# Kernel optimization log

Measured on AMD Instinct MI355X. Metric: run time of the kernel, lower is better.

The kernel has to match this reference:

```python
import jax, jax.numpy as jnp
import numpy as np

B, T, D = 2, 1024, 2048
E, K, H = 64, 4, 512          # n_experts, top-k, expert_dim
S, HS = 2, H * K              # shared experts, shared hidden dim
CAP = 512


def setup_inputs() -> dict:
    key = jax.random.key(0)
    ks = jax.random.split(key, 9)
    scale = 0.02
    return {
        "x": jax.random.normal(ks[0], (B, T, D), jnp.float32),
        "Wr": jax.random.normal(ks[1], (D, E), jnp.float32) * scale,
        "router_bias": jnp.zeros((E,), jnp.float32),
        "Wg": jax.random.normal(ks[2], (E, D, H), jnp.float32) * scale,
        "Wu": jax.random.normal(ks[3], (E, D, H), jnp.float32) * scale,
        "Wd": jax.random.normal(ks[4], (E, H, D), jnp.float32) * scale,
        "Sg": jax.random.normal(ks[5], (S, D, HS), jnp.float32) * scale,
        "Su": jax.random.normal(ks[6], (S, D, HS), jnp.float32) * scale,
        "Sd": jax.random.normal(ks[7], (S, HS, D), jnp.float32) * scale,
    }


def reference(x, Wr, router_bias, Wg, Wu, Wd, Sg, Su, Sd):
    Bx, Tx, Dx = x.shape
    N = Bx * Tx
    flat = x.reshape(N, Dx)                              # [N, D]

    # ---- router ----
    logits = flat @ Wr + router_bias                     # [N, E]
    scores = jax.nn.softmax(logits, axis=-1)
    topk_scores, topk_idx = jax.lax.top_k(scores, K)     # [N, K]
    topk_scores = topk_scores / topk_scores.sum(-1, keepdims=True)

    eid = topk_idx.reshape(-1)                           # [N*K] expert per assignment
    w = topk_scores.reshape(-1)                          # [N*K] combine weight
    tok = jnp.repeat(jnp.arange(N), K)                   # [N*K] source token id

    # position of each assignment within its expert's buffer
    oh = jax.nn.one_hot(eid, E, dtype=jnp.int32)         # [N*K, E]
    pos = ((jnp.cumsum(oh, axis=0) * oh).sum(-1) - 1)    # [N*K]
    valid = pos < CAP

    # ---- dispatch: scatter tokens into per-expert buffers ----
    xb = jnp.zeros((E, CAP, Dx), x.dtype).at[eid, pos].set(flat[tok], mode="drop")

    # ---- grouped SwiGLU expert FFN ----
    h = jax.nn.silu(jnp.einsum("ecd,edh->ech", xb, Wg)) * jnp.einsum("ecd,edh->ech", xb, Wu)
    yb = jnp.einsum("ech,ehd->ecd", h, Wd)               # [E, CAP, D]

    # ---- combine: gather back and weighted scatter-add to tokens ----
    y = yb[eid, jnp.minimum(pos, CAP - 1)] * (w * valid)[:, None]
    out = jnp.zeros((N, Dx), x.dtype).at[tok].add(y)

    # ---- always-on shared experts ----
    hs = jax.nn.silu(jnp.einsum("nd,sdh->nsh", flat, Sg)) * jnp.einsum("nd,sdh->nsh", flat, Su)
    out = out + jnp.einsum("nsh,shd->nd", hs, Sd)

    return out.reshape(Bx, Tx, Dx)
```

## Files before the change

### kernel.cpp

```cpp
#include <hip/hip_runtime.h>
#include <hip/hip_bf16.h>
#include <stdint.h>

#define N_TOK 2048
#define DM    2048
#define NEXP  64
#define TOPK  4
#define HEXP  512
#define CAPC  512
#define NSH   2
#define HSH   2048
#define RTB   8

typedef __attribute__((ext_vector_type(8))) short short8;
typedef __attribute__((ext_vector_type(4))) short short4v;
typedef __attribute__((ext_vector_type(4))) float f32x4;
typedef __attribute__((ext_vector_type(4))) float f4;

static __device__ __forceinline__ unsigned short f2bf(float f) {
  union { float f; unsigned u; } v; v.f = f;
  unsigned r = v.u + 0x7FFFu + ((v.u >> 16) & 1u);
  return (unsigned short)(r >> 16);
}

__global__ __launch_bounds__(256) void k_convert(const float* __restrict__ x,
                                                 unsigned short* __restrict__ xb) {
  int i = (blockIdx.x * 256 + threadIdx.x) * 8;
  f4 a = *(const f4*)(x + i);
  f4 b = *(const f4*)(x + i + 4);
  short8 o;
  o[0]=f2bf(a[0]); o[1]=f2bf(a[1]); o[2]=f2bf(a[2]); o[3]=f2bf(a[3]);
  o[4]=f2bf(b[0]); o[5]=f2bf(b[1]); o[6]=f2bf(b[2]); o[7]=f2bf(b[3]);
  *(short8*)(xb + i) = o;
}

#define ARGMAX_ROUND(S,I)                                            \
  { float bv = v; int bi = lane;                                     \
    _Pragma("unroll")                                                \
    for (int o = 32; o; o >>= 1) {                                   \
      float ov = __shfl_xor(bv, o); int oi = __shfl_xor(bi, o);      \
      if (ov > bv || (ov == bv && oi < bi)) { bv = ov; bi = oi; }    \
    }                                                                \
    S = bv; I = bi; if (lane == bi) v = -1.f; }

__global__ __launch_bounds__(256) void k_router(const float* __restrict__ x,
    const float* __restrict__ Wr, const float* __restrict__ bias,
    int* __restrict__ cnt, int* __restrict__ lists, float* __restrict__ wlist) {
  __shared__ float part[4][RTB][64];
  __shared__ float logits[RTB][64];
  int t = threadIdx.x;
  int e = t & 63, sl = t >> 6;
  int tok0 = blockIdx.x * RTB;
  const float* xp = x + (size_t)tok0 * DM;
  float acc[RTB];
#pragma unroll
  for (int i = 0; i < RTB; ++i) acc[i] = 0.f;
  for (int d = sl * 512; d < sl * 512 + 512; ++d) {
    float w = Wr[(size_t)d * NEXP + e];
#pragma unroll
    for (int i = 0; i < RTB; ++i) acc[i] += xp[(size_t)i * DM + d] * w;
  }
#pragma unroll
  for (int i = 0; i < RTB; ++i) part[sl][i][e] = acc[i];
  __syncthreads();
  for (int i = sl; i < RTB; i += 4)
    logits[i][e] = part[0][i][e] + part[1][i][e] + part[2][i][e] + part[3][i][e] + bias[e];
  __syncthreads();
  int lane = t & 63, wv = t >> 6;
  for (int i = wv * 2; i < wv * 2 + 2; ++i) {
    float lg = logits[i][lane];
    float m = lg;
#pragma unroll
    for (int o = 32; o; o >>= 1) m = fmaxf(m, __shfl_xor(m, o));
    float p = expf(lg - m);
    float sm = p;
#pragma unroll
    for (int o = 32; o; o >>= 1) sm += __shfl_xor(sm, o);
    float v = p / sm;
    float s0, s1, s2, s3; int i0, i1, i2, i3;
    ARGMAX_ROUND(s0, i0)
    ARGMAX_ROUND(s1, i1)
    ARGMAX_ROUND(s2, i2)
    ARGMAX_ROUND(s3, i3)
    float tot = s0 + s1 + s2 + s3;
    if (lane < TOPK) {
      float myw = (lane == 0 ? s0 : lane == 1 ? s1 : lane == 2 ? s2 : s3) / tot;
      int   mye = (lane == 0 ? i0 : lane == 1 ? i1 : lane == 2 ? i2 : i3);
      int pos = atomicAdd(&cnt[mye], 1);
      if (pos < CAPC) {
        lists[mye * CAPC + pos] = tok0 + i;
        wlist[mye * CAPC + pos] = myw;
      }
    }
  }
}

__global__ void k_offs(const int* __restrict__ cnt, int* __restrict__ offs) {
  int l = threadIdx.x;
  int c = min(cnt[l], CAPC);
  int sum = c;
#pragma unroll
  for (int o = 1; o < 64; o <<= 1) {
    int ov = __shfl_up(sum, o);
    if (l >= o) sum += ov;
  }
  offs[l + 1] = sum;
  if (l == 0) offs[0] = 0;
}


template<bool GATHER>
static __device__ __forceinline__ void loadA(const unsigned short* __restrict__ src,
    int lda, int m0, int Mvalid, const int* __restrict__ gl, int k0, short8 (&r)[4]) {
  int tid = threadIdx.x;
#pragma unroll
  for (int p = 0; p < 4; ++p) {
    int idx = p * 256 + tid;
    int row = idx >> 3;
    int ko  = (idx & 7) * 8;
    int grow = m0 + row;
    if (grow < Mvalid) {
      int srow = GATHER ? gl[grow] : grow;
      r[p] = *(const short8*)(src + (size_t)srow * lda + k0 + ko);
    } else {
#pragma unroll
      for (int j = 0; j < 8; ++j) r[p][j] = 0;
    }
  }
}

static __device__ __forceinline__ void writeA(const short8 (&r)[4], unsigned short* lA) {
  int tid = threadIdx.x;
#pragma unroll
  for (int p = 0; p < 4; ++p) {
    int idx = p * 256 + tid;
    int row = idx >> 3;
    int ko  = (idx & 7) * 8;
    int byte = row * 128 + ko * 2;
    byte ^= (row & 7) << 4;
    *(short8*)((char*)lA + byte) = r[p];
  }
}

static __device__ __forceinline__ void loadB(const float* __restrict__ B, int ldb,
    int k0, int n0, f4 (&r)[4]) {
  int tid = threadIdx.x;
  int kb = tid >> 4;
  int nb = tid & 15;
  const float* p = B + (size_t)(k0 + kb * 4) * ldb + n0 + nb * 4;
#pragma unroll
  for (int q = 0; q < 4; ++q) r[q] = *(const f4*)(p + (size_t)q * ldb);
}

static __device__ __forceinline__ void writeB(const f4 (&r)[4], unsigned short* lB) {
  int tid = threadIdx.x;
  int kb = tid >> 4;
  int nb = tid & 15;
#pragma unroll
  for (int c = 0; c < 4; ++c) {
    short4v vv;
    vv[0] = (short)f2bf(r[0][c]); vv[1] = (short)f2bf(r[1][c]);
    vv[2] = (short)f2bf(r[2][c]); vv[3] = (short)f2bf(r[3][c]);
    int n = nb * 4 + c;
    int byte = n * 128 + kb * 8;
    byte ^= (n & 7) << 4;
    *(short4v*)((char*)lB + byte) = vv;
  }
}

static __device__ __forceinline__ short8 frag_ld(const unsigned short* lds, int row, int kElem) {
  int byte = row * 128 + kElem * 2;
  byte ^= (row & 7) << 4;
  return *(const short8*)((const char*)lds + byte);
}

static __device__ __forceinline__ void mma1(const unsigned short* lA, const unsigned short* lB,
    f32x4 (&acc)[4][2], int wm, int wn, int lane) {
  int r16 = lane & 15;
  int kg  = (lane >> 4) * 8;
#pragma unroll
  for (int kk = 0; kk < 2; ++kk) {
    int kb = kk * 32 + kg;
    short8 a[4], b[2];
#pragma unroll
    for (int mf = 0; mf < 4; ++mf) a[mf] = frag_ld(lA, wm + mf * 16 + r16, kb);
#pragma unroll
    for (int nf = 0; nf < 2; ++nf) b[nf] = frag_ld(lB, wn + nf * 16 + r16, kb);
#pragma unroll
    for (int mf = 0; mf < 4; ++mf)
#pragma unroll
      for (int nf = 0; nf < 2; ++nf)
        acc[mf][nf] = __builtin_amdgcn_mfma_f32_16x16x32_bf16(a[mf], b[nf], acc[mf][nf], 0, 0, 0);
  }
}

static __device__ __forceinline__ void mma2(const unsigned short* lA,
    const unsigned short* lBg, const unsigned short* lBu,
    f32x4 (&accg)[4][2], f32x4 (&accu)[4][2], int wm, int wn, int lane) {
  int r16 = lane & 15;
  int kg  = (lane >> 4) * 8;
#pragma unroll
  for (int kk = 0; kk < 2; ++kk) {
    int kb = kk * 32 + kg;
    short8 a[4], bg[2], bu[2];
#pragma unroll
    for (int mf = 0; mf < 4; ++mf) a[mf] = frag_ld(lA, wm + mf * 16 + r16, kb);
#pragma unroll
    for (int nf = 0; nf < 2; ++nf) {
      bg[nf] = frag_ld(lBg, wn + nf * 16 + r16, kb);
      bu[nf] = frag_ld(lBu, wn + nf * 16 + r16, kb);
    }
#pragma unroll
    for (int mf = 0; mf < 4; ++mf)
#pragma unroll
      for (int nf = 0; nf < 2; ++nf) {
        accg[mf][nf] = __builtin_amdgcn_mfma_f32_16x16x32_bf16(a[mf], bg[nf], accg[mf][nf], 0, 0, 0);
        accu[mf][nf] = __builtin_amdgcn_mfma_f32_16x16x32_bf16(a[mf], bu[nf], accu[mf][nf], 0, 0, 0);
      }
  }
}

static __device__ __forceinline__ float silu_mul(float g, float u) {
  return g / (1.f + expf(-g)) * u;
}

__global__ __launch_bounds__(256) void k_expert_gateup(const unsigned short* __restrict__ xbf,
    const float* __restrict__ Wg, const float* __restrict__ Wu,
    const int* __restrict__ cnt, const int* __restrict__ offs,
    const int* __restrict__ lists, unsigned short* __restrict__ hws) {
  int e = blockIdx.y;
  int ne = min(cnt[e], CAPC);
  if (ne == 0) return;
  int n0 = blockIdx.x * 64;
  const float* Bg = Wg + (size_t)e * DM * HEXP;
  const float* Bu = Wu + (size_t)e * DM * HEXP;
  const int* lst = lists + e * CAPC;
  int base = offs[e];
  __shared__ unsigned short lA[128 * 64];
  __shared__ unsigned short lBg[64 * 64];
  __shared__ unsigned short lBu[64 * 64];
  int lane = threadIdx.x & 63, wv = threadIdx.x >> 6;
  int wm = (wv >> 1) * 64, wn = (wv & 1) * 32;
  for (int m0 = 0; m0 < ne; m0 += 128) {
    f32x4 accg[4][2] = {};
    f32x4 accu[4][2] = {};
    short8 ra[4]; f4 rg[4], ru[4];
    loadA<true>(xbf, DM, m0, ne, lst, 0, ra);
    loadB(Bg, HEXP, 0, n0, rg);
    loadB(Bu, HEXP, 0, n0, ru);
    for (int k0 = 0; k0 < DM; k0 += 64) {
      writeA(ra, lA);
      writeB(rg, lBg);
      writeB(ru, lBu);
      int kn = k0 + 64;
      if (kn < DM) {
        loadA<true>(xbf, DM, m0, ne, lst, kn, ra);
        loadB(Bg, HEXP, kn, n0, rg);
        loadB(Bu, HEXP, kn, n0, ru);
      }
      __syncthreads();
      mma2(lA, lBg, lBu, accg, accu, wm, wn, lane);
      __syncthreads();
    }
#pragma unroll
    for (int mf = 0; mf < 4; ++mf)
#pragma unroll
      for (int r = 0; r < 4; ++r) {
        int rl = m0 + wm + mf * 16 + (lane >> 4) * 4 + r;
        if (rl < ne) {
#pragma unroll
          for (int nf = 0; nf < 2; ++nf) {
            int col = n0 + wn + nf * 16 + (lane & 15);
            float h = silu_mul(accg[mf][nf][r], accu[mf][nf][r]);
            hws[(size_t)(base + rl) * HEXP + col] = f2bf(h);
          }
        }
      }
  }
}

__global__ __launch_bounds__(256) void k_shared_gateup(const unsigned short* __restrict__ xbf,
    const float* __restrict__ Sg, const float* __restrict__ Su,
    unsigned short* __restrict__ hs) {
  int n0 = blockIdx.x * 64;
  int m0 = blockIdx.y * 128;
  int s  = blockIdx.z;
  const float* Bg = Sg + (size_t)s * DM * HSH;
  const float* Bu = Su + (size_t)s * DM * HSH;
  __shared__ unsigned short lA[128 * 64];
  __shared__ unsigned short lBg[64 * 64];
  __shared__ unsigned short lBu[64 * 64];
  int lane = threadIdx.x & 63, wv = threadIdx.x >> 6;
  int wm = (wv >> 1) * 64, wn = (wv & 1) * 32;
  f32x4 accg[4][2] = {};
  f32x4 accu[4][2] = {};
  short8 ra[4]; f4 rg[4], ru[4];
  loadA<false>(xbf, DM, m0, N_TOK, nullptr, 0, ra);
  loadB(Bg, HSH, 0, n0, rg);
  loadB(Bu, HSH, 0, n0, ru);
  for (int k0 = 0; k0 < DM; k0 += 64) {
    writeA(ra, lA);
    writeB(rg, lBg);
    writeB(ru, lBu);
    int kn = k0 + 64;
    if (kn < DM) {
      loadA<false>(xbf, DM, m0, N_TOK, nullptr, kn, ra);
      loadB(Bg, HSH, kn, n0, rg);
      loadB(Bu, HSH, kn, n0, ru);
    }
    __syncthreads();
    mma2(lA, lBg, lBu, accg, accu, wm, wn, lane);
    __syncthreads();
  }
#pragma unroll
  for (int mf = 0; mf < 4; ++mf)
#pragma unroll
    for (int nf = 0; nf < 2; ++nf)
#pragma unroll
      for (int r = 0; r < 4; ++r) {
        int row = m0 + wm + mf * 16 + (lane >> 4) * 4 + r;
        int col = n0 + wn + nf * 16 + (lane & 15);
        float h = silu_mul(accg[mf][nf][r], accu[mf][nf][r]);
        hs[(size_t)row * (NSH * HSH) + s * HSH + col] = f2bf(h);
      }
}

__global__ __launch_bounds__(256) void k_shared_down(const unsigned short* __restrict__ hs,
    const float* __restrict__ Sd, float* __restrict__ out) {
  int n0 = blockIdx.x * 64;
  int m0 = blockIdx.y * 128;
  __shared__ unsigned short lA[128 * 64];
  __shared__ unsigned short lB[64 * 64];
  int lane = threadIdx.x & 63, wv = threadIdx.x >> 6;
  int wm = (wv >> 1) * 64, wn = (wv & 1) * 32;
  f32x4 acc[4][2] = {};
  short8 ra[4]; f4 rb[4];
  loadA<false>(hs, NSH * HSH, m0, N_TOK, nullptr, 0, ra);
  loadB(Sd, DM, 0, n0, rb);
  for (int k0 = 0; k0 < NSH * HSH; k0 += 64) {
    writeA(ra, lA);
    writeB(rb, lB);
    int kn = k0 + 64;
    if (kn < NSH * HSH) {
      loadA<false>(hs, NSH * HSH, m0, N_TOK, nullptr, kn, ra);
      loadB(Sd, DM, kn, n0, rb);
    }
    __syncthreads();
    mma1(lA, lB, acc, wm, wn, lane);
    __syncthreads();
  }
#pragma unroll
  for (int mf = 0; mf < 4; ++mf)
#pragma unroll
    for (int nf = 0; nf < 2; ++nf)
#pragma unroll
      for (int r = 0; r < 4; ++r) {
        int row = m0 + wm + mf * 16 + (lane >> 4) * 4 + r;
        int col = n0 + wn + nf * 16 + (lane & 15);
        out[(size_t)row * DM + col] = acc[mf][nf][r];
      }
}

__global__ __launch_bounds__(256) void k_expert_down(const unsigned short* __restrict__ hws,
    const float* __restrict__ Wd, const int* __restrict__ cnt, const int* __restrict__ offs,
    const int* __restrict__ lists, const float* __restrict__ wlist,
    float* __restrict__ out) {
  int e = blockIdx.y;
  int ne = min(cnt[e], CAPC);
  if (ne == 0) return;
  int n0 = blockIdx.x * 64;
  const float* B = Wd + (size_t)e * HEXP * DM;
  const unsigned short* A = hws + (size_t)offs[e] * HEXP;
  __shared__ unsigned short lA[128 * 64];
  __shared__ unsigned short lB[64 * 64];
  int lane = threadIdx.x & 63, wv = threadIdx.x >> 6;
  int wm = (wv >> 1) * 64, wn = (wv & 1) * 32;
  for (int m0 = 0; m0 < ne; m0 += 128) {
    f32x4 acc[4][2] = {};
    short8 ra[4]; f4 rb[4];
    loadA<false>(A, HEXP, m0, ne, nullptr, 0, ra);
    loadB(B, DM, 0, n0, rb);
    for (int k0 = 0; k0 < HEXP; k0 += 64) {
      writeA(ra, lA);
      writeB(rb, lB);
      int kn = k0 + 64;
      if (kn < HEXP) {
        loadA<false>(A, HEXP, m0, ne, nullptr, kn, ra);
        loadB(B, DM, kn, n0, rb);
      }
      __syncthreads();
      mma1(lA, lB, acc, wm, wn, lane);
      __syncthreads();
    }
#pragma unroll
    for (int mf = 0; mf < 4; ++mf)
#pragma unroll
      for (int r = 0; r < 4; ++r) {
        int rl = m0 + wm + mf * 16 + (lane >> 4) * 4 + r;
        if (rl < ne) {
          int tok  = lists[e * CAPC + rl];
          float w  = wlist[e * CAPC + rl];
#pragma unroll
          for (int nf = 0; nf < 2; ++nf) {
            int col = n0 + wn + nf * 16 + (lane & 15);
            atomicAdd(out + (size_t)tok * DM + col, acc[mf][nf][r] * w);
          }
        }
      }
  }
}

extern "C" void kernel_launch(void* const* d_in, const int* in_sizes, int n_in,
                              void* d_out, int out_size, void* d_ws, size_t ws_size,
                              hipStream_t stream) {
  const float* x    = (const float*)d_in[0];
  const float* Wr   = (const float*)d_in[1];
  const float* bias = (const float*)d_in[2];
  const float* Wg   = (const float*)d_in[3];
  const float* Wu   = (const float*)d_in[4];
  const float* Wd   = (const float*)d_in[5];
  const float* Sg   = (const float*)d_in[6];
  const float* Su   = (const float*)d_in[7];
  const float* Sd   = (const float*)d_in[8];
  float* out = (float*)d_out;
  char* ws = (char*)d_ws;

  const size_t off_cnt   = 0;
  const size_t off_offs  = 256;
  const size_t off_lists = 1024;
  const size_t off_wlist = off_lists + (size_t)NEXP * CAPC * 4;
  const size_t off_xbf   = off_wlist + (size_t)NEXP * CAPC * 4;
  const size_t off_hs    = off_xbf + (size_t)N_TOK * DM * 2;
  const size_t off_h     = off_hs + (size_t)N_TOK * NSH * HSH * 2;
  const size_t req       = off_h + (size_t)N_TOK * TOPK * HEXP * 2;
  if (ws_size < req) return;

  int* cnt            = (int*)(ws + off_cnt);
  int* offs           = (int*)(ws + off_offs);
  int* lists          = (int*)(ws + off_lists);
  float* wlist        = (float*)(ws + off_wlist);
  unsigned short* xbf = (unsigned short*)(ws + off_xbf);
  unsigned short* hs  = (unsigned short*)(ws + off_hs);
  unsigned short* hws = (unsigned short*)(ws + off_h);

  hipMemsetAsync(cnt, 0, NEXP * sizeof(int), stream);
  k_convert<<<(N_TOK * DM) / (256 * 8), 256, 0, stream>>>(x, xbf);
  k_router<<<N_TOK / RTB, 256, 0, stream>>>(x, Wr, bias, cnt, lists, wlist);
  k_offs<<<1, 64, 0, stream>>>(cnt, offs);
  k_expert_gateup<<<dim3(HEXP / 64, NEXP), 256, 0, stream>>>(xbf, Wg, Wu, cnt, offs, lists, hws);
  k_shared_gateup<<<dim3(HSH / 64, N_TOK / 128, NSH), 256, 0, stream>>>(xbf, Sg, Su, hs);
  k_shared_down<<<dim3(DM / 64, N_TOK / 128), 256, 0, stream>>>(hs, Sd, out);
  k_expert_down<<<dim3(DM / 64, NEXP), 256, 0, stream>>>(hws, Wd, cnt, offs, lists, wlist, out);
}
```

Measured before the change: 669.4 us.

## Double-buffer LDS tiles in all four GEMM kernels to halve barriers

Converts the single-buffered LDS tiles in the expert and shared gate/up and down kernels to ping-pong buffers. Each k-step now needs one barrier instead of two, and the LDS writes for the next tile overlap the MFMA work on the current one. The barrier is a custom inline asm that waits only on lgkmcnt before s_barrier, which doubles LDS usage per block and may reduce occupancy.

```diff
diff --git a/kernel.cpp b/kernel.cpp
--- a/kernel.cpp
+++ b/kernel.cpp
@@ -16,6 +16,8 @@
 typedef __attribute__((ext_vector_type(4))) short short4v;
 typedef __attribute__((ext_vector_type(4))) float f32x4;
 typedef __attribute__((ext_vector_type(4))) float f4;
+
+#define LGKM_BAR() asm volatile("s_waitcnt lgkmcnt(0)\n\ts_barrier" ::: "memory")
 
 static __device__ __forceinline__ unsigned short f2bf(float f) {
   union { float f; unsigned u; } v; v.f = f;
@@ -236,9 +238,9 @@
   const float* Bu = Wu + (size_t)e * DM * HEXP;
   const int* lst = lists + e * CAPC;
   int base = offs[e];
-  __shared__ unsigned short lA[128 * 64];
-  __shared__ unsigned short lBg[64 * 64];
-  __shared__ unsigned short lBu[64 * 64];
+  __shared__ unsigned short lA[2][128 * 64];
+  __shared__ unsigned short lBg[2][64 * 64];
+  __shared__ unsigned short lBu[2][64 * 64];
   int lane = threadIdx.x & 63, wv = threadIdx.x >> 6;
   int wm = (wv >> 1) * 64, wn = (wv & 1) * 32;
   for (int m0 = 0; m0 < ne; m0 += 128) {
@@ -248,19 +250,31 @@
     loadA<true>(xbf, DM, m0, ne, lst, 0, ra);
     loadB(Bg, HEXP, 0, n0, rg);
     loadB(Bu, HEXP, 0, n0, ru);
-    for (int k0 = 0; k0 < DM; k0 += 64) {
-      writeA(ra, lA);
-      writeB(rg, lBg);
-      writeB(ru, lBu);
-      int kn = k0 + 64;
-      if (kn < DM) {
-        loadA<true>(xbf, DM, m0, ne, lst, kn, ra);
-        loadB(Bg, HEXP, kn, n0, rg);
-        loadB(Bu, HEXP, kn, n0, ru);
-      }
-      __syncthreads();
-      mma2(lA, lBg, lBu, accg, accu, wm, wn, lane);
-      __syncthreads();
+    writeA(ra, lA[0]); writeB(rg, lBg[0]); writeB(ru, lBu[0]);
+    loadA<true>(xbf, DM, m0, ne, lst, 64, ra);
+    loadB(Bg, HEXP, 64, n0, rg);
+    loadB(Bu, HEXP, 64, n0, ru);
+    LGKM_BAR();
+#pragma unroll 1
+    for (int k0 = 0; k0 < DM; k0 += 128) {
+      mma2(lA[0], lBg[0], lBu[0], accg, accu, wm, wn, lane);
+      writeA(ra, lA[1]); writeB(rg, lBg[1]); writeB(ru, lBu[1]);
+      if (k0 + 128 < DM) {
+        loadA<true>(xbf, DM, m0, ne, lst, k0 + 128, ra);
+        loadB(Bg, HEXP, k0 + 128, n0, rg);
+        loadB(Bu, HEXP, k0 + 128, n0, ru);
+      }
+      LGKM_BAR();
+      mma2(lA[1], lBg[1], lBu[1], accg, accu, wm, wn, lane);
+      if (k0 + 128 < DM) {
+        writeA(ra, lA[0]); writeB(rg, lBg[0]); writeB(ru, lBu[0]);
+        if (k0 + 192 < DM) {
+          loadA<true>(xbf, DM, m0, ne, lst, k0 + 192, ra);
+          loadB(Bg, HEXP, k0 + 192, n0, rg);
+          loadB(Bu, HEXP, k0 + 192, n0, ru);
+        }
+      }
+      LGKM_BAR();
     }
 #pragma unroll
     for (int mf = 0; mf < 4; ++mf)
@@ -287,9 +301,9 @@
   int s  = blockIdx.z;
   const float* Bg = Sg + (size_t)s * DM * HSH;
   const float* Bu = Su + (size_t)s * DM * HSH;
-  __shared__ unsigned short lA[128 * 64];
-  __shared__ unsigned short lBg[64 * 64];
-  __shared__ unsigned short lBu[64 * 64];
+  __shared__ unsigned short lA[2][128 * 64];
+  __shared__ unsigned short lBg[2][64 * 64];
+  __shared__ unsigned short lBu[2][64 * 64];
   int lane = threadIdx.x & 63, wv = threadIdx.x >> 6;
   int wm = (wv >> 1) * 64, wn = (wv & 1) * 32;
   f32x4 accg[4][2] = {};
@@ -298,19 +312,31 @@
   loadA<false>(xbf, DM, m0, N_TOK, nullptr, 0, ra);
   loadB(Bg, HSH, 0, n0, rg);
   loadB(Bu, HSH, 0, n0, ru);
-  for (int k0 = 0; k0 < DM; k0 += 64) {
-    writeA(ra, lA);
-    writeB(rg, lBg);
-    writeB(ru, lBu);
-    int kn = k0 + 64;
-    if (kn < DM) {
-      loadA<false>(xbf, DM, m0, N_TOK, nullptr, kn, ra);
-      loadB(Bg, HSH, kn, n0, rg);
-      loadB(Bu, HSH, kn, n0, ru);
-    }
-    __syncthreads();
-    mma2(lA, lBg, lBu, accg, accu, wm, wn, lane);
-    __syncthreads();
+  writeA(ra, lA[0]); writeB(rg, lBg[0]); writeB(ru, lBu[0]);
+  loadA<false>(xbf, DM, m0, N_TOK, nullptr, 64, ra);
+  loadB(Bg, HSH, 64, n0, rg);
+  loadB(Bu, HSH, 64, n0, ru);
+  LGKM_BAR();
+#pragma unroll 1
+  for (int k0 = 0; k0 < DM; k0 += 128) {
+    mma2(lA[0], lBg[0], lBu[0], accg, accu, wm, wn, lane);
+    writeA(ra, lA[1]); writeB(rg, lBg[1]); writeB(ru, lBu[1]);
+    if (k0 + 128 < DM) {
+      loadA<false>(xbf, DM, m0, N_TOK, nullptr, k0 + 128, ra);
+      loadB(Bg, HSH, k0 + 128, n0, rg);
+      loadB(Bu, HSH, k0 + 128, n0, ru);
+    }
+    LGKM_BAR();
+    mma2(lA[1], lBg[1], lBu[1], accg, accu, wm, wn, lane);
+    if (k0 + 128 < DM) {
+      writeA(ra, lA[0]); writeB(rg, lBg[0]); writeB(ru, lBu[0]);
+      if (k0 + 192 < DM) {
+        loadA<false>(xbf, DM, m0, N_TOK, nullptr, k0 + 192, ra);
+        loadB(Bg, HSH, k0 + 192, n0, rg);
+        loadB(Bu, HSH, k0 + 192, n0, ru);
+      }
+    }
+    LGKM_BAR();
   }
 #pragma unroll
   for (int mf = 0; mf < 4; ++mf)
@@ -329,25 +355,36 @@
     const float* __restrict__ Sd, float* __restrict__ out) {
   int n0 = blockIdx.x * 64;
   int m0 = blockIdx.y * 128;
-  __shared__ unsigned short lA[128 * 64];
-  __shared__ unsigned short lB[64 * 64];
+  __shared__ unsigned short lA[2][128 * 64];
+  __shared__ unsigned short lB[2][64 * 64];
   int lane = threadIdx.x & 63, wv = threadIdx.x >> 6;
   int wm = (wv >> 1) * 64, wn = (wv & 1) * 32;
   f32x4 acc[4][2] = {};
   short8 ra[4]; f4 rb[4];
   loadA<false>(hs, NSH * HSH, m0, N_TOK, nullptr, 0, ra);
   loadB(Sd, DM, 0, n0, rb);
-  for (int k0 = 0; k0 < NSH * HSH; k0 += 64) {
-    writeA(ra, lA);
-    writeB(rb, lB);
-    int kn = k0 + 64;
-    if (kn < NSH * HSH) {
-      loadA<false>(hs, NSH * HSH, m0, N_TOK, nullptr, kn, ra);
-      loadB(Sd, DM, kn, n0, rb);
-    }
-    __syncthreads();
-    mma1(lA, lB, acc, wm, wn, lane);
-    __syncthreads();
+  writeA(ra, lA[0]); writeB(rb, lB[0]);
+  loadA<false>(hs, NSH * HSH, m0, N_TOK, nullptr, 64, ra);
+  loadB(Sd, DM, 64, n0, rb);
+  LGKM_BAR();
+#pragma unroll 1
+  for (int k0 = 0; k0 < NSH * HSH; k0 += 128) {
+    mma1(lA[0], lB[0], acc, wm, wn, lane);
+    writeA(ra, lA[1]); writeB(rb, lB[1]);
+    if (k0 + 128 < NSH * HSH) {
+      loadA<false>(hs, NSH * HSH, m0, N_TOK, nullptr, k0 + 128, ra);
+      loadB(Sd, DM, k0 + 128, n0, rb);
+    }
+    LGKM_BAR();
+    mma1(lA[1], lB[1], acc, wm, wn, lane);
+    if (k0 + 128 < NSH * HSH) {
+      writeA(ra, lA[0]); writeB(rb, lB[0]);
+      if (k0 + 192 < NSH * HSH) {
+        loadA<false>(hs, NSH * HSH, m0, N_TOK, nullptr, k0 + 192, ra);
+        loadB(Sd, DM, k0 + 192, n0, rb);
+      }
+    }
+    LGKM_BAR();
   }
 #pragma unroll
   for (int mf = 0; mf < 4; ++mf)
@@ -371,8 +408,8 @@
   int n0 = blockIdx.x * 64;
   const float* B = Wd + (size_t)e * HEXP * DM;
   const unsigned short* A = hws + (size_t)offs[e] * HEXP;
-  __shared__ unsigned short lA[128 * 64];
-  __shared__ unsigned short lB[64 * 64];
+  __shared__ unsigned short lA[2][128 * 64];
+  __shared__ unsigned short lB[2][64 * 64];
   int lane = threadIdx.x & 63, wv = threadIdx.x >> 6;
   int wm = (wv >> 1) * 64, wn = (wv & 1) * 32;
   for (int m0 = 0; m0 < ne; m0 += 128) {
@@ -380,17 +417,28 @@
     short8 ra[4]; f4 rb[4];
     loadA<false>(A, HEXP, m0, ne, nullptr, 0, ra);
     loadB(B, DM, 0, n0, rb);
-    for (int k0 = 0; k0 < HEXP; k0 += 64) {
-      writeA(ra, lA);
-      writeB(rb, lB);
-      int kn = k0 + 64;
-      if (kn < HEXP) {
-        loadA<false>(A, HEXP, m0, ne, nullptr, kn, ra);
-        loadB(B, DM, kn, n0, rb);
-      }
-      __syncthreads();
-      mma1(lA, lB, acc, wm, wn, lane);
-      __syncthreads();
+    writeA(ra, lA[0]); writeB(rb, lB[0]);
+    loadA<false>(A, HEXP, m0, ne, nullptr, 64, ra);
+    loadB(B, DM, 64, n0, rb);
+    LGKM_BAR();
+#pragma unroll 1
+    for (int k0 = 0; k0 < HEXP; k0 += 128) {
+      mma1(lA[0], lB[0], acc, wm, wn, lane);
+      writeA(ra, lA[1]); writeB(rb, lB[1]);
+      if (k0 + 128 < HEXP) {
+        loadA<false>(A, HEXP, m0, ne, nullptr, k0 + 128, ra);
+        loadB(B, DM, k0 + 128, n0, rb);
+      }
+      LGKM_BAR();
+      mma1(lA[1], lB[1], acc, wm, wn, lane);
+      if (k0 + 128 < HEXP) {
+        writeA(ra, lA[0]); writeB(rb, lB[0]);
+        if (k0 + 192 < HEXP) {
+          loadA<false>(A, HEXP, m0, ne, nullptr, k0 + 192, ra);
+          loadB(B, DM, k0 + 192, n0, rb);
+        }
+      }
+      LGKM_BAR();
     }
 #pragma unroll
     for (int mf = 0; mf < 4; ++mf)
```

New measurement: 721.8 us. +7.8%, slower.
